# Kernel tuning notes

Measured on AMD Instinct MI355X. Metric: run time of the kernel, lower is better.

Reference implementation:

```python
import jax, jax.numpy as jnp
import numpy as np

# static config (matches init_kwargs and a standard 4-level FPN for ~800px input)
SPATIAL_SHAPES = ((100, 100), (50, 50), (25, 25), (13, 13))  # (H_l, W_l)
B, C, H, L, P = 2, 256, 8, 4, 4
DFFN = 2048
DH = C // H
LQ = sum(h * w for h, w in SPATIAL_SHAPES)  # 13294


def layer_norm(x, g, b, eps=1e-5):
    m = jnp.mean(x, -1, keepdims=True)
    v = jnp.mean((x - m) ** 2, -1, keepdims=True)
    return (x - m) * jax.lax.rsqrt(v + eps) * g + b


def ms_deform_sample(value, loc, attn):
    # value [B,Lv,H,DH], loc [B,Lq,H,L,P,2] in [0,1], attn [B,Lq,H,L,P]
    value = jnp.transpose(value, (0, 2, 1, 3))  # [B,H,Lv,DH]
    lq = loc.shape[1]
    out = jnp.zeros((B, H, lq, DH), value.dtype)
    start = 0
    for l, (Hl, Wl) in enumerate(SPATIAL_SHAPES):
        v = jax.lax.dynamic_slice_in_dim(value, start, Hl * Wl, axis=2)  # [B,H,N_l,DH]
        # grid_sample(align_corners=False) coords: x = loc_x*W - 0.5
        gx = jnp.transpose(loc[:, :, :, l, :, 0], (0, 2, 1, 3)) * Wl - 0.5  # [B,H,Lq,P]
        gy = jnp.transpose(loc[:, :, :, l, :, 1], (0, 2, 1, 3)) * Hl - 0.5
        aw = jnp.transpose(attn[:, :, :, l, :], (0, 2, 1, 3))  # [B,H,Lq,P]
        x0 = jnp.floor(gx)
        y0 = jnp.floor(gy)
        for dx in (0.0, 1.0):
            for dy in (0.0, 1.0):
                xi = x0 + dx
                yi = y0 + dy
                w = (1.0 - jnp.abs(gx - xi)) * (1.0 - jnp.abs(gy - yi))
                valid = (xi >= 0) & (xi < Wl) & (yi >= 0) & (yi < Hl)
                idx = (jnp.clip(yi, 0, Hl - 1) * Wl + jnp.clip(xi, 0, Wl - 1)).astype(jnp.int32)
                g = jnp.take_along_axis(v, idx.reshape(B, H, -1)[..., None], axis=2)  # [B,H,Lq*P,DH]
                ww = (w * aw * valid.astype(w.dtype))[..., None]  # [B,H,Lq,P,1]
                out = out + jnp.sum(g.reshape(B, H, lq, P, DH) * ww, axis=3)
        start += Hl * Wl
    return jnp.transpose(out, (0, 2, 1, 3)).reshape(B, lq, C)


def setup_inputs() -> dict:
    key = jax.random.key(0)
    ks = jax.random.split(key, 16)
    s = 0.02
    return {
        "src": jax.random.normal(ks[0], (B, LQ, C), jnp.float32),
        "pos": jax.random.normal(ks[1], (B, LQ, C), jnp.float32),
        "reference_points": jax.random.uniform(ks[2], (B, LQ, L, 2), jnp.float32),
        "w_value": jax.random.normal(ks[3], (C, C), jnp.float32) * s,
        "b_value": jnp.zeros((C,), jnp.float32),
        "w_off": jax.random.normal(ks[4], (C, H * L * P * 2), jnp.float32) * s,
        "b_off": jax.random.normal(ks[5], (H * L * P * 2,), jnp.float32) * s,
        "w_attn": jax.random.normal(ks[6], (C, H * L * P), jnp.float32) * s,
        "b_attn": jnp.zeros((H * L * P,), jnp.float32),
        "w_out": jax.random.normal(ks[7], (C, C), jnp.float32) * s,
        "b_out": jnp.zeros((C,), jnp.float32),
        "ln1_g": jnp.ones((C,), jnp.float32),
        "ln1_b": jnp.zeros((C,), jnp.float32),
        "w_ffn1": jax.random.normal(ks[8], (C, DFFN), jnp.float32) * s,
        "b_ffn1": jnp.zeros((DFFN,), jnp.float32),
        "w_ffn2": jax.random.normal(ks[9], (DFFN, C), jnp.float32) * s,
        "b_ffn2": jnp.zeros((C,), jnp.float32),
        "ln2_g": jnp.ones((C,), jnp.float32),
        "ln2_b": jnp.zeros((C,), jnp.float32),
    }


def reference(src, pos, reference_points, w_value, b_value, w_off, b_off, w_attn, b_attn,
              w_out, b_out, ln1_g, ln1_b, w_ffn1, b_ffn1, w_ffn2, b_ffn2, ln2_g, ln2_b):
    # DeformableTransformerEncoderLayer.forward (eval mode, no dropout)
    q = src + pos  # with_pos_embed
    lq = q.shape[1]
    value = (src @ w_value + b_value).reshape(B, -1, H, DH)
    off = (q @ w_off + b_off).reshape(B, lq, H, L, P, 2)
    attn = (q @ w_attn + b_attn).reshape(B, lq, H, L * P)
    attn = jax.nn.softmax(attn, axis=-1).reshape(B, lq, H, L, P)
    # offset_normalizer = (W_l, H_l)
    norm = jnp.array([[w, h] for h, w in SPATIAL_SHAPES], dtype=src.dtype)
    loc = reference_points[:, :, None, :, None, :] + off / norm[None, None, None, :, None, :]
    src2 = ms_deform_sample(value, loc, attn) @ w_out + b_out
    x = layer_norm(src + src2, ln1_g, ln1_b)
    ff = jax.nn.relu(x @ w_ffn1 + b_ffn1) @ w_ffn2 + b_ffn2
    return layer_norm(x + ff, ln2_g, ln2_b)
```

## Files before the change

kernel.cpp:

```cpp
#include <hip/hip_runtime.h>

#define LQN   13294
#define NBAT  2
#define MROWS (NBAT * LQN)
#define CCH   256
#define NHEAD 8
#define DHEAD 32
#define NLVL  4
#define NPT   4
#define DFF   2048

typedef short short8 __attribute__((ext_vector_type(8)));
typedef float f32x4 __attribute__((ext_vector_type(4)));
typedef unsigned short u16;
typedef u16 u16x4 __attribute__((ext_vector_type(4)));

__device__ __forceinline__ u16 f2bf(float f) {
  unsigned int u = __builtin_bit_cast(unsigned int, f);
  u += 0x7fffu + ((u >> 16) & 1u);
  return (u16)(u >> 16);
}
__device__ __forceinline__ float bf2f(u16 s) {
  unsigned int u = ((unsigned int)s) << 16;
  return __builtin_bit_cast(float, u);
}
__device__ __forceinline__ void async16(const void* g, void* l) {
  __builtin_amdgcn_global_load_lds(
      (const __attribute__((address_space(1))) void*)g,
      (__attribute__((address_space(3))) void*)l, 16, 0, 0);
}

__global__ __launch_bounds__(256, 2)
void gemm_dual(const u16* __restrict__ A0, const u16* __restrict__ BT0,
               const float* __restrict__ bias0, u16* __restrict__ C0,
               const u16* __restrict__ A1, const u16* __restrict__ BT1,
               const float* __restrict__ bias1, float* __restrict__ C1)
{
  __shared__ u16 As[2][128 * 64];
  __shared__ u16 Bs[2][128 * 64];
  const int t    = threadIdx.x;
  const int lane = t & 63;
  const int wid  = t >> 6;
  const int wm   = wid >> 1, wn = wid & 1;
  const int bm   = blockIdx.x;
  const int bnG  = blockIdx.y;
  const bool first = bnG < 2;
  const u16* A    = first ? A0 : A1;
  const u16* BT   = first ? BT0 : BT1;
  const float* bias = first ? bias0 : bias1;
  const int  bn   = first ? bnG : bnG - 2;
  const int l15  = lane & 15;
  const int kq   = lane >> 4;

  f32x4 acc[4][4];
#pragma unroll
  for (int m = 0; m < 4; ++m)
#pragma unroll
    for (int n = 0; n < 4; ++n) acc[m][n] = (f32x4)0.0f;

  auto stage = [&](int buf, int kt) {
#pragma unroll
    for (int i = 0; i < 4; ++i) {
      const int c   = i * 256 + t;
      const int row = c >> 3;
      const int kg  = (c & 7) ^ (row & 7);
      int ar = bm * 128 + row; ar = ar < MROWS ? ar : MROWS - 1;
      async16(&A[(size_t)ar * 256 + kt + kg * 8], &As[buf][c * 8]);
      const int br = bn * 128 + row;
      async16(&BT[(size_t)br * 256 + kt + kg * 8], &Bs[buf][c * 8]);
    }
  };

  stage(0, 0);
  __syncthreads();
  int cur = 0;

  for (int kt = 0; kt < 256; kt += 64) {
    if (kt + 64 < 256) stage(cur ^ 1, kt + 64);

#pragma unroll
    for (int kk = 0; kk < 2; ++kk) {
      short8 af[4], bfr[4];
#pragma unroll
      for (int m = 0; m < 4; ++m) {
        const int row = wm * 64 + m * 16 + l15;
        const int xb  = (kk * 64 + kq * 16) ^ ((row & 7) << 4);
        af[m] = *(const short8*)((const char*)&As[cur][0] + row * 128 + xb);
      }
#pragma unroll
      for (int n = 0; n < 4; ++n) {
        const int col = wn * 64 + n * 16 + l15;
        const int xb  = (kk * 64 + kq * 16) ^ ((col & 7) << 4);
        bfr[n] = *(const short8*)((const char*)&Bs[cur][0] + col * 128 + xb);
      }
#pragma unroll
      for (int m = 0; m < 4; ++m)
#pragma unroll
        for (int n = 0; n < 4; ++n)
          acc[m][n] = __builtin_amdgcn_mfma_f32_16x16x32_bf16(af[m], bfr[n], acc[m][n], 0, 0, 0);
    }

    __syncthreads();
    cur ^= 1;
  }

  const int crow0 = bm * 128 + wm * 64;
  const int ccol0 = bn * 128 + wn * 64;
#pragma unroll
  for (int n = 0; n < 4; ++n) {
    int col = ccol0 + n * 16 + l15;
    float bv = bias[col];
#pragma unroll
    for (int m = 0; m < 4; ++m) {
      int rbase = crow0 + m * 16 + kq * 4;
#pragma unroll
      for (int j = 0; j < 4; ++j) {
        int row = rbase + j;
        if (row < MROWS) {
          float v = acc[m][n][j] + bv;
          if (first) C0[(size_t)row * 256 + col] = f2bf(v);
          else       C1[(size_t)row * 384 + col] = v;
        }
      }
    }
  }
}

__global__ __launch_bounds__(512, 1)
void outproj_ln1(const u16* __restrict__ src2_bf, const u16* __restrict__ WT_out,
                 const float* __restrict__ b_out, const float* __restrict__ src,
                 const float* __restrict__ g1, const float* __restrict__ be1,
                 float* __restrict__ x_f32, u16* __restrict__ x_bf)
{
  extern __shared__ char smem[];
  char* As0 = smem;
  char* As1 = smem + 16384;
  char* Bs0 = smem + 32768;
  char* Bs1 = smem + 65536;
  float2* red = (float2*)(smem + 98304);

  const int t    = threadIdx.x;
  const int lane = t & 63;
  const int wid  = t >> 6;
  const int wm   = wid >> 2, wn = wid & 3;
  const int l15  = lane & 15;
  const int kq   = lane >> 4;
  const int bm   = blockIdx.x;

  auto stage = [&](char* Abuf, char* Bbuf, int kt) {
#pragma unroll
    for (int i = 0; i < 2; ++i) {
      const int c   = i * 512 + t;
      const int row = c >> 3;
      const int kg  = (c & 7) ^ (row & 7);
      int ar = bm * 128 + row; ar = ar < MROWS ? ar : MROWS - 1;
      async16(&src2_bf[(size_t)ar * 256 + kt + kg * 8], Abuf + c * 16);
    }
#pragma unroll
    for (int i = 0; i < 4; ++i) {
      const int c   = i * 512 + t;
      const int row = c >> 3;
      const int kg  = (c & 7) ^ (row & 7);
      async16(&WT_out[(size_t)row * 256 + kt + kg * 8], Bbuf + c * 16);
    }
  };

  f32x4 acc[4][4];
#pragma unroll
  for (int m = 0; m < 4; ++m)
#pragma unroll
    for (int n = 0; n < 4; ++n) acc[m][n] = (f32x4)0.0f;

  stage(As0, Bs0, 0);
  __syncthreads();

  for (int kt = 0; kt < 256; kt += 64) {
    const int cur = (kt >> 6) & 1;
    char* Ause = cur ? As1 : As0;
    char* Buse = cur ? Bs1 : Bs0;
    if (kt + 64 < 256) stage(cur ? As0 : As1, cur ? Bs0 : Bs1, kt + 64);

#pragma unroll
    for (int kk = 0; kk < 2; ++kk) {
      short8 af[4], bfr[4];
#pragma unroll
      for (int m = 0; m < 4; ++m) {
        const int row = wm * 64 + m * 16 + l15;
        const int xb  = (kk * 64 + kq * 16) ^ ((row & 7) << 4);
        af[m] = *(const short8*)(Ause + row * 128 + xb);
      }
#pragma unroll
      for (int n = 0; n < 4; ++n) {
        const int col = wn * 64 + n * 16 + l15;
        const int xb  = (kk * 64 + kq * 16) ^ ((col & 7) << 4);
        bfr[n] = *(const short8*)(Buse + col * 128 + xb);
      }
#pragma unroll
      for (int m = 0; m < 4; ++m)
#pragma unroll
        for (int n = 0; n < 4; ++n)
          acc[m][n] = __builtin_amdgcn_mfma_f32_16x16x32_bf16(af[m], bfr[n], acc[m][n], 0, 0, 0);
    }
    __syncthreads();
  }

#pragma unroll
  for (int n = 0; n < 4; ++n) {
    const int col = wn * 64 + n * 16 + l15;
    const float bv = b_out[col];
#pragma unroll
    for (int m = 0; m < 4; ++m)
#pragma unroll
      for (int j = 0; j < 4; ++j) {
        int row = bm * 128 + wm * 64 + m * 16 + kq * 4 + j;
        row = row < MROWS ? row : MROWS - 1;
        acc[m][n][j] += bv + src[(size_t)row * 256 + col];
      }
  }
  float s1[4][4], s2[4][4];
#pragma unroll
  for (int m = 0; m < 4; ++m)
#pragma unroll
    for (int j = 0; j < 4; ++j) {
      float a = 0.f, b = 0.f;
#pragma unroll
      for (int n = 0; n < 4; ++n) { const float v = acc[m][n][j]; a += v; b += v * v; }
      s1[m][j] = a; s2[m][j] = b;
    }
#pragma unroll
  for (int o = 1; o < 16; o <<= 1)
#pragma unroll
    for (int m = 0; m < 4; ++m)
#pragma unroll
      for (int j = 0; j < 4; ++j) {
        s1[m][j] += __shfl_xor(s1[m][j], o, 64);
        s2[m][j] += __shfl_xor(s2[m][j], o, 64);
      }
  if (l15 == 0)
#pragma unroll
    for (int m = 0; m < 4; ++m)
#pragma unroll
      for (int j = 0; j < 4; ++j)
        red[(wm * 64 + m * 16 + kq * 4 + j) * 4 + wn] = make_float2(s1[m][j], s2[m][j]);
  __syncthreads();
  float mean[4][4], rstd[4][4];
#pragma unroll
  for (int m = 0; m < 4; ++m)
#pragma unroll
    for (int j = 0; j < 4; ++j) {
      const int rl = wm * 64 + m * 16 + kq * 4 + j;
      float a = 0.f, b = 0.f;
#pragma unroll
      for (int w = 0; w < 4; ++w) { const float2 r = red[rl * 4 + w]; a += r.x; b += r.y; }
      const float mu = a * (1.0f / 256.0f);
      mean[m][j] = mu;
      rstd[m][j] = rsqrtf(b * (1.0f / 256.0f) - mu * mu + 1e-5f);
    }
#pragma unroll
  for (int n = 0; n < 4; ++n) {
    const int col = wn * 64 + n * 16 + l15;
    const float gg = g1[col], bb = be1[col];
#pragma unroll
    for (int m = 0; m < 4; ++m)
#pragma unroll
      for (int j = 0; j < 4; ++j) {
        const int row = bm * 128 + wm * 64 + m * 16 + kq * 4 + j;
        if (row < MROWS) {
          const float y = (acc[m][n][j] - mean[m][j]) * rstd[m][j] * gg + bb;
          x_f32[(size_t)row * 256 + col] = y;
          x_bf[(size_t)row * 256 + col] = f2bf(y);
        }
      }
  }
}

__global__ __launch_bounds__(1024, 2)
void ffn_ln2(const u16* __restrict__ x_bf, const u16* __restrict__ W1T,
             const u16* __restrict__ W2T, const float* __restrict__ b1,
             const float* __restrict__ b2, const float* __restrict__ x_f32,
             const float* __restrict__ g2, const float* __restrict__ be2,
             float* __restrict__ out)
{
  extern __shared__ char smem[];
  u16*  w1s = (u16*)(smem);
  u16*  w2s = (u16*)(smem + 65536);
  char* ps  = smem + 131072;
  float2* red = (float2*)(smem + 149504);

  const int t    = threadIdx.x;
  const int lane = t & 63;
  const int wid  = t >> 6;
  const int l15  = lane & 15;
  const int kq   = lane >> 4;
  const int bm   = blockIdx.x;
  const int pwm  = wid >> 1, pwn = wid & 1;
  const int vwm  = wid >> 2, vwn = wid & 3;

  short8 xr[8];
  {
    int ar = bm * 128 + pwm * 16 + l15;
    ar = ar < MROWS ? ar : MROWS - 1;
    const char* xb = (const char*)x_bf + (size_t)ar * 512 + kq * 16;
#pragma unroll
    for (int ks = 0; ks < 8; ++ks) xr[ks] = *(const short8*)(xb + ks * 64);
  }

  auto stage = [&](int buf, int it) {
#pragma unroll
    for (int i = 0; i < 2; ++i) {
      const int c  = i * 1024 + t;
      const int r1 = c >> 5;
      const int k1 = ((c & 31) ^ (r1 & 7)) * 8;
      async16(&W1T[(size_t)(it * 64 + r1) * 256 + k1], &w1s[buf * 16384 + c * 8]);
      const int r2 = c >> 3;
      const int k2 = ((c & 7) ^ (r2 & 7)) * 8;
      async16(&W2T[(size_t)r2 * 2048 + it * 64 + k2], &w2s[buf * 16384 + c * 8]);
    }
  };

  f32x4 acc[2][4];
#pragma unroll
  for (int m = 0; m < 2; ++m)
#pragma unroll
    for (int n = 0; n < 4; ++n) acc[m][n] = (f32x4)0.0f;

  stage(0, 0);
  __syncthreads();

  for (int it = 0; it < 32; ++it) {
    const int cur = it & 1;
    if (it < 31) stage(cur ^ 1, it + 1);

    f32x4 p[2];
    p[0] = (f32x4)0.0f; p[1] = (f32x4)0.0f;
#pragma unroll
    for (int ks = 0; ks < 8; ++ks) {
#pragma unroll
      for (int n = 0; n < 2; ++n) {
        const int wrow = pwn * 32 + n * 16 + l15;
        const int xb   = (((ks * 4 + kq) ^ (wrow & 7)) << 4);
        const short8 bfr = *(const short8*)((const char*)&w1s[cur * 16384] + wrow * 512 + xb);
        p[n] = __builtin_amdgcn_mfma_f32_16x16x32_bf16(xr[ks], bfr, p[n], 0, 0, 0);
      }
    }

#pragma unroll
    for (int n = 0; n < 2; ++n) {
      const int col = pwn * 32 + n * 16 + l15;
      const float bv = b1[it * 64 + col];
#pragma unroll
      for (int j = 0; j < 4; ++j) {
        const int prow = pwm * 16 + kq * 4 + j;
        *(u16*)(ps + prow * 144 + col * 2) = f2bf(fmaxf(p[n][j] + bv, 0.0f));
      }
    }
    __syncthreads();

#pragma unroll
    for (int kk = 0; kk < 2; ++kk) {
      short8 paf[2];
#pragma unroll
      for (int m = 0; m < 2; ++m) {
        const int arow = vwm * 32 + m * 16 + l15;
        paf[m] = *(const short8*)(ps + arow * 144 + (kk * 4 + kq) * 16);
      }
#pragma unroll
      for (int n = 0; n < 4; ++n) {
        const int brow = vwn * 64 + n * 16 + l15;
        const int xb   = (((kk * 4 + kq) ^ (brow & 7)) << 4);
        const short8 bfr = *(const short8*)((const char*)&w2s[cur * 16384] + brow * 128 + xb);
#pragma unroll
        for (int m = 0; m < 2; ++m)
          acc[m][n] = __builtin_amdgcn_mfma_f32_16x16x32_bf16(paf[m], bfr, acc[m][n], 0, 0, 0);
      }
    }
    __syncthreads();
  }

#pragma unroll
  for (int n = 0; n < 4; ++n) {
    const int col = vwn * 64 + n * 16 + l15;
    const float bv = b2[col];
#pragma unroll
    for (int m = 0; m < 2; ++m)
#pragma unroll
      for (int j = 0; j < 4; ++j) {
        int row = bm * 128 + vwm * 32 + m * 16 + kq * 4 + j;
        row = row < MROWS ? row : MROWS - 1;
        acc[m][n][j] += bv + x_f32[(size_t)row * 256 + col];
      }
  }
  float s1[2][4], s2[2][4];
#pragma unroll
  for (int m = 0; m < 2; ++m)
#pragma unroll
    for (int j = 0; j < 4; ++j) {
      float a = 0.f, b = 0.f;
#pragma unroll
      for (int n = 0; n < 4; ++n) { const float v = acc[m][n][j]; a += v; b += v * v; }
      s1[m][j] = a; s2[m][j] = b;
    }
#pragma unroll
  for (int o = 1; o < 16; o <<= 1)
#pragma unroll
    for (int m = 0; m < 2; ++m)
#pragma unroll
      for (int j = 0; j < 4; ++j) {
        s1[m][j] += __shfl_xor(s1[m][j], o, 64);
        s2[m][j] += __shfl_xor(s2[m][j], o, 64);
      }
  if (l15 == 0)
#pragma unroll
    for (int m = 0; m < 2; ++m)
#pragma unroll
      for (int j = 0; j < 4; ++j)
        red[(vwm * 32 + m * 16 + kq * 4 + j) * 4 + vwn] = make_float2(s1[m][j], s2[m][j]);
  __syncthreads();
  float mean[2][4], rstd[2][4];
#pragma unroll
  for (int m = 0; m < 2; ++m)
#pragma unroll
    for (int j = 0; j < 4; ++j) {
      const int rl = vwm * 32 + m * 16 + kq * 4 + j;
      float a = 0.f, b = 0.f;
#pragma unroll
      for (int w = 0; w < 4; ++w) { const float2 r = red[rl * 4 + w]; a += r.x; b += r.y; }
      const float mu = a * (1.0f / 256.0f);
      mean[m][j] = mu;
      rstd[m][j] = rsqrtf(b * (1.0f / 256.0f) - mu * mu + 1e-5f);
    }
#pragma unroll
  for (int n = 0; n < 4; ++n) {
    const int col = vwn * 64 + n * 16 + l15;
    const float gg = g2[col], bb = be2[col];
#pragma unroll
    for (int m = 0; m < 2; ++m)
#pragma unroll
      for (int j = 0; j < 4; ++j) {
        const int row = bm * 128 + vwm * 32 + m * 16 + kq * 4 + j;
        if (row < MROWS)
          out[(size_t)row * 256 + col] = (acc[m][n][j] - mean[m][j]) * rstd[m][j] * gg + bb;
      }
  }
}

__global__ __launch_bounds__(256)
void sampler_kernel(const float* __restrict__ offattn,
                    const float* __restrict__ refp,
                    const u16*  __restrict__ value,
                    u16*        __restrict__ src2)
{
  __shared__ float2 sWI[4][8][65];

  const int t    = threadIdx.x;
  const int r4   = t >> 6;
  const int lane = t & 63;
  const int row  = blockIdx.x * 4 + r4;
  const int b    = row / LQN;

  {
    const float* oa = offattn + (size_t)row * 384;
    const float* rp = refp + (size_t)row * 8;
    const int p16 = lane & 15;
    const int l   = p16 >> 2;
    const int Wl  = (l == 0) ? 100 : (l == 1) ? 50 : (l == 2) ? 25 : 13;
    const int st  = (l == 0) ? 0 : (l == 1) ? 10000 : (l == 2) ? 12500 : 13125;
    const float rx = rp[l * 2 + 0] * (float)Wl - 0.5f;
    const float ry = rp[l * 2 + 1] * (float)Wl - 0.5f;

#pragma unroll
    for (int s = 0; s < 2; ++s) {
      const int h = s * 4 + (lane >> 4);
      float logit = oa[256 + h * 16 + p16];
      float mx = logit;
#pragma unroll
      for (int o = 1; o < 16; o <<= 1) mx = fmaxf(mx, __shfl_xor(mx, o, 64));
      float e = __expf(logit - mx);
      float ssum = e;
#pragma unroll
      for (int o = 1; o < 16; o <<= 1) ssum += __shfl_xor(ssum, o, 64);
      const float aw = e / ssum;

      const float ox = oa[(h * 16 + p16) * 2 + 0];
      const float oy = oa[(h * 16 + p16) * 2 + 1];
      const float gx = rx + ox;
      const float gy = ry + oy;
      const float x0f = floorf(gx), y0f = floorf(gy);
      const int   x0 = (int)x0f, y0 = (int)y0f;
      const float fx = gx - x0f, fy = gy - y0f;
#pragma unroll
      for (int c = 0; c < 4; ++c) {
        const int dx = c & 1, dy = c >> 1;
        const int xi = x0 + dx, yi = y0 + dy;
        const float wx = dx ? fx : 1.0f - fx;
        const float wy = dy ? fy : 1.0f - fy;
        const bool valid = (xi >= 0) && (xi < Wl) && (yi >= 0) && (yi < Wl);
        const int xc = min(max(xi, 0), Wl - 1);
        const int yc = min(max(yi, 0), Wl - 1);
        const int idx = st + yc * Wl + xc;
        const float w = wx * wy * aw * (valid ? 1.0f : 0.0f);
        sWI[r4][h][p16 * 4 + c] = make_float2(w, __builtin_bit_cast(float, idx));
      }
    }
  }
  __syncthreads();

  {
    const int h  = lane >> 3;
    const int c4 = lane & 7;
    const char* vbase = (const char*)value + (size_t)b * LQN * 512 + h * 64 + c4 * 8;
    const float2* wi = sWI[r4][h];

    float a0 = 0.f, a1 = 0.f, a2 = 0.f, a3 = 0.f;
#pragma unroll 16
    for (int e = 0; e < 64; ++e) {
      const float2 p = wi[e];
      const float w  = p.x;
      const int  idx = __builtin_bit_cast(int, p.y);
      const unsigned long long u = *(const unsigned long long*)(vbase + (size_t)idx * 512);
      a0 += w * bf2f((u16)(u));
      a1 += w * bf2f((u16)(u >> 16));
      a2 += w * bf2f((u16)(u >> 32));
      a3 += w * bf2f((u16)(u >> 48));
    }
    u16x4 o;
    o[0] = f2bf(a0); o[1] = f2bf(a1); o[2] = f2bf(a2); o[3] = f2bf(a3);
    *(u16x4*)&src2[(size_t)row * 256 + h * 32 + c4 * 4] = o;
  }
}

__global__ __launch_bounds__(256)
void prep_qsrc(const float* __restrict__ src, const float* __restrict__ pos,
               u16* __restrict__ src_bf, u16* __restrict__ q_bf)
{
  const size_t i = (size_t)blockIdx.x * 256 + threadIdx.x;
  const f32x4 s = ((const f32x4*)src)[i];
  const f32x4 p = ((const f32x4*)pos)[i];
  u16x4 sb, qb;
#pragma unroll
  for (int j = 0; j < 4; ++j) { sb[j] = f2bf(s[j]); qb[j] = f2bf(s[j] + p[j]); }
  ((u16x4*)src_bf)[i] = sb;
  ((u16x4*)q_bf)[i]   = qb;
}

__global__ __launch_bounds__(256)
void prep_weights(const float* __restrict__ w_value, const float* __restrict__ w_off,
                  const float* __restrict__ w_attn,  const float* __restrict__ w_out,
                  const float* __restrict__ w_ffn1,  const float* __restrict__ w_ffn2,
                  const float* __restrict__ b_off,   const float* __restrict__ b_attn,
                  u16* __restrict__ WT_val, u16* __restrict__ WT_oa, u16* __restrict__ WT_out,
                  u16* __restrict__ WT_f1,  u16* __restrict__ WT_f2, float* __restrict__ bias_oa)
{
  int i = blockIdx.x * 256 + threadIdx.x;
  if (i < 65536) {
    const int k = i >> 8, n = i & 255;
    WT_val[n * 256 + k] = f2bf(w_value[i]);
  } else if ((i -= 65536) < 65536) {
    const int k = i >> 8, n = i & 255;
    WT_oa[n * 256 + k] = f2bf(w_off[i]);
  } else if ((i -= 65536) < 32768) {
    const int k = i >> 7, n = i & 127;
    WT_oa[(256 + n) * 256 + k] = f2bf(w_attn[i]);
  } else if ((i -= 32768) < 65536) {
    const int k = i >> 8, n = i & 255;
    WT_out[n * 256 + k] = f2bf(w_out[i]);
  } else if ((i -= 65536) < 524288) {
    const int k = i >> 11, n = i & 2047;
    WT_f1[n * 256 + k] = f2bf(w_ffn1[i]);
  } else if ((i -= 524288) < 524288) {
    const int k = i >> 8, n = i & 255;
    WT_f2[n * 2048 + k] = f2bf(w_ffn2[i]);
  } else if ((i -= 524288) < 384) {
    bias_oa[i] = (i < 256) ? b_off[i] : b_attn[i - 256];
  }
}

extern "C" void kernel_launch(void* const* d_in, const int* in_sizes, int n_in,
                              void* d_out, int out_size, void* d_ws, size_t ws_size,
                              hipStream_t stream)
{
  const float* src     = (const float*)d_in[0];
  const float* pos     = (const float*)d_in[1];
  const float* refp    = (const float*)d_in[2];
  const float* w_value = (const float*)d_in[3];
  const float* b_value = (const float*)d_in[4];
  const float* w_off   = (const float*)d_in[5];
  const float* b_off   = (const float*)d_in[6];
  const float* w_attn  = (const float*)d_in[7];
  const float* b_attn  = (const float*)d_in[8];
  const float* w_out   = (const float*)d_in[9];
  const float* b_out   = (const float*)d_in[10];
  const float* ln1_g   = (const float*)d_in[11];
  const float* ln1_b   = (const float*)d_in[12];
  const float* w_ffn1  = (const float*)d_in[13];
  const float* b_ffn1  = (const float*)d_in[14];
  const float* w_ffn2  = (const float*)d_in[15];
  const float* b_ffn2  = (const float*)d_in[16];
  const float* ln2_g   = (const float*)d_in[17];
  const float* ln2_b   = (const float*)d_in[18];

  char* ws = (char*)d_ws;
  size_t off = 0;
  auto alloc = [&](size_t bytes) { void* p = ws + off; off += (bytes + 255) & ~(size_t)255; return p; };

  u16*   src_bf   = (u16*)  alloc((size_t)MROWS * 256 * 2);
  u16*   q_bf     = (u16*)  alloc((size_t)MROWS * 256 * 2);
  float* offattn  = (float*)alloc((size_t)MROWS * 384 * 4);
  u16*   value_bf = (u16*)  alloc((size_t)MROWS * 256 * 2);
  u16*   src2_bf  = (u16*)  alloc((size_t)MROWS * 256 * 2);
  float* x_f32    = (float*)alloc((size_t)MROWS * 256 * 4);
  u16*   WT_val   = (u16*)  alloc(256 * 256 * 2);
  u16*   WT_oa    = (u16*)  alloc(384 * 256 * 2);
  u16*   WT_out   = (u16*)  alloc(256 * 256 * 2);
  u16*   WT_f1    = (u16*)  alloc(2048 * 256 * 2);
  u16*   WT_f2    = (u16*)  alloc((size_t)256 * 2048 * 2);
  float* bias_oa  = (float*)alloc(384 * 4);

  u16* x_bf = q_bf;

  prep_weights<<<4994, 256, 0, stream>>>(w_value, w_off, w_attn, w_out, w_ffn1, w_ffn2,
                                         b_off, b_attn,
                                         WT_val, WT_oa, WT_out, WT_f1, WT_f2, bias_oa);

  prep_qsrc<<<6647, 256, 0, stream>>>(src, pos, src_bf, q_bf);

  static bool attr_set = false;
  if (!attr_set) {
    hipFuncSetAttribute((const void*)ffn_ln2,
                        hipFuncAttributeMaxDynamicSharedMemorySize, 153600);
    hipFuncSetAttribute((const void*)outproj_ln1,
                        hipFuncAttributeMaxDynamicSharedMemorySize, 102400);
    attr_set = true;
  }

  gemm_dual<<<dim3(208, 5), 256, 0, stream>>>(src_bf, WT_val, b_value, value_bf,
                                              q_bf, WT_oa, bias_oa, offattn);

  sampler_kernel<<<MROWS / 4, 256, 0, stream>>>(offattn, refp, value_bf, src2_bf);

  outproj_ln1<<<208, 512, 102400, stream>>>(src2_bf, WT_out, b_out, src,
                                            ln1_g, ln1_b, x_f32, x_bf);

  ffn_ln2<<<208, 1024, 153600, stream>>>(x_bf, WT_f1, WT_f2, b_ffn1, b_ffn2,
                                         x_f32, ln2_g, ln2_b, (float*)d_out);
}
```

Before: 239.0 us.

## Restructure FFN kernel into software-pipelined 512-thread loop with 4-stage weight buffers

The fused FFN+LN2 kernel now runs 512 threads per block instead of 1024, so each wave holds twice the rows of accumulators. It walks the hidden dimension in 64 chunks of 32 instead of 32 chunks of 64. Weights are staged through a 4-deep ring with prefetch two chunks ahead. The hidden activations are double-buffered, so the FFN2 MFMAs for chunk it-1 and the FFN1 MFMAs for chunk it share one barrier per iteration instead of two. The intent is to cut barrier stalls and overlap the two GEMM stages, at the cost of higher register pressure, lower occupancy and an unswizzled W2 tile layout that may cause LDS bank conflicts.

```diff
diff --git a/kernel.cpp b/kernel.cpp
--- a/kernel.cpp
+++ b/kernel.cpp
@@ -274,7 +274,7 @@
   }
 }
 
-__global__ __launch_bounds__(1024, 2)
+__global__ __launch_bounds__(512)
 void ffn_ln2(const u16* __restrict__ x_bf, const u16* __restrict__ W1T,
              const u16* __restrict__ W2T, const float* __restrict__ b1,
              const float* __restrict__ b2, const float* __restrict__ x_f32,
@@ -282,10 +282,10 @@
              float* __restrict__ out)
 {
   extern __shared__ char smem[];
-  u16*  w1s = (u16*)(smem);
-  u16*  w2s = (u16*)(smem + 65536);
+  char* w1s = smem;
+  char* w2s = smem + 65536;
   char* ps  = smem + 131072;
-  float2* red = (float2*)(smem + 149504);
+  float2* red = (float2*)(smem + 151552);
 
   const int t    = threadIdx.x;
   const int lane = t & 63;
@@ -296,85 +296,106 @@
   const int pwm  = wid >> 1, pwn = wid & 1;
   const int vwm  = wid >> 2, vwn = wid & 3;
 
-  short8 xr[8];
-  {
-    int ar = bm * 128 + pwm * 16 + l15;
+  short8 xr[2][8];
+#pragma unroll
+  for (int m = 0; m < 2; ++m) {
+    int ar = bm * 128 + pwm * 32 + m * 16 + l15;
     ar = ar < MROWS ? ar : MROWS - 1;
     const char* xb = (const char*)x_bf + (size_t)ar * 512 + kq * 16;
 #pragma unroll
-    for (int ks = 0; ks < 8; ++ks) xr[ks] = *(const short8*)(xb + ks * 64);
+    for (int ks = 0; ks < 8; ++ks) xr[m][ks] = *(const short8*)(xb + ks * 64);
   }
 
   auto stage = [&](int buf, int it) {
 #pragma unroll
     for (int i = 0; i < 2; ++i) {
-      const int c  = i * 1024 + t;
+      const int c  = i * 512 + t;
       const int r1 = c >> 5;
       const int k1 = ((c & 31) ^ (r1 & 7)) * 8;
-      async16(&W1T[(size_t)(it * 64 + r1) * 256 + k1], &w1s[buf * 16384 + c * 8]);
-      const int r2 = c >> 3;
-      const int k2 = ((c & 7) ^ (r2 & 7)) * 8;
-      async16(&W2T[(size_t)r2 * 2048 + it * 64 + k2], &w2s[buf * 16384 + c * 8]);
+      async16(&W1T[(size_t)(it * 32 + r1) * 256 + k1], w1s + buf * 16384 + c * 16);
+      const int r2 = c >> 2;
+      const int k2 = (c & 3) * 8;
+      async16(&W2T[(size_t)r2 * 2048 + it * 32 + k2], w2s + buf * 16384 + c * 16);
     }
   };
 
-  f32x4 acc[2][4];
-#pragma unroll
-  for (int m = 0; m < 2; ++m)
+  f32x4 acc[4][4];
+#pragma unroll
+  for (int m = 0; m < 4; ++m)
 #pragma unroll
     for (int n = 0; n < 4; ++n) acc[m][n] = (f32x4)0.0f;
 
   stage(0, 0);
+  stage(1, 1);
   __syncthreads();
 
-  for (int it = 0; it < 32; ++it) {
-    const int cur = it & 1;
-    if (it < 31) stage(cur ^ 1, it + 1);
-
-    f32x4 p[2];
-    p[0] = (f32x4)0.0f; p[1] = (f32x4)0.0f;
-#pragma unroll
-    for (int ks = 0; ks < 8; ++ks) {
-#pragma unroll
-      for (int n = 0; n < 2; ++n) {
-        const int wrow = pwn * 32 + n * 16 + l15;
-        const int xb   = (((ks * 4 + kq) ^ (wrow & 7)) << 4);
-        const short8 bfr = *(const short8*)((const char*)&w1s[cur * 16384] + wrow * 512 + xb);
-        p[n] = __builtin_amdgcn_mfma_f32_16x16x32_bf16(xr[ks], bfr, p[n], 0, 0, 0);
-      }
-    }
-
-#pragma unroll
-    for (int n = 0; n < 2; ++n) {
-      const int col = pwn * 32 + n * 16 + l15;
-      const float bv = b1[it * 64 + col];
-#pragma unroll
-      for (int j = 0; j < 4; ++j) {
-        const int prow = pwm * 16 + kq * 4 + j;
-        *(u16*)(ps + prow * 144 + col * 2) = f2bf(fmaxf(p[n][j] + bv, 0.0f));
-      }
-    }
-    __syncthreads();
-
-#pragma unroll
-    for (int kk = 0; kk < 2; ++kk) {
-      short8 paf[2];
-#pragma unroll
-      for (int m = 0; m < 2; ++m) {
-        const int arow = vwm * 32 + m * 16 + l15;
-        paf[m] = *(const short8*)(ps + arow * 144 + (kk * 4 + kq) * 16);
+  for (int it = 0; it < 64; ++it) {
+    if (it + 2 < 64) stage((it + 2) & 3, it + 2);
+
+    if (it > 0) {
+      const char* psR = ps + ((it - 1) & 1) * 10240;
+      const char* w2u = w2s + ((it - 1) & 3) * 16384;
+      short8 paf[4];
+#pragma unroll
+      for (int m = 0; m < 4; ++m) {
+        const int arow = vwm * 64 + m * 16 + l15;
+        paf[m] = *(const short8*)(psR + arow * 80 + kq * 16);
       }
 #pragma unroll
       for (int n = 0; n < 4; ++n) {
         const int brow = vwn * 64 + n * 16 + l15;
-        const int xb   = (((kk * 4 + kq) ^ (brow & 7)) << 4);
-        const short8 bfr = *(const short8*)((const char*)&w2s[cur * 16384] + brow * 128 + xb);
+        const short8 bfr = *(const short8*)(w2u + brow * 64 + kq * 16);
+#pragma unroll
+        for (int m = 0; m < 4; ++m)
+          acc[m][n] = __builtin_amdgcn_mfma_f32_16x16x32_bf16(paf[m], bfr, acc[m][n], 0, 0, 0);
+      }
+    }
+
+    {
+      const char* w1u = w1s + (it & 3) * 16384;
+      char* psW = ps + (it & 1) * 10240;
+      f32x4 p[2];
+      p[0] = (f32x4)0.0f; p[1] = (f32x4)0.0f;
+#pragma unroll
+      for (int ks = 0; ks < 8; ++ks) {
+        const int wrow = pwn * 16 + l15;
+        const int xb   = (((ks * 4 + kq) ^ (wrow & 7)) << 4);
+        const short8 bfr = *(const short8*)(w1u + wrow * 512 + xb);
 #pragma unroll
         for (int m = 0; m < 2; ++m)
-          acc[m][n] = __builtin_amdgcn_mfma_f32_16x16x32_bf16(paf[m], bfr, acc[m][n], 0, 0, 0);
-      }
-    }
+          p[m] = __builtin_amdgcn_mfma_f32_16x16x32_bf16(xr[m][ks], bfr, p[m], 0, 0, 0);
+      }
+      const int col = pwn * 16 + l15;
+      const float bv = b1[it * 32 + col];
+#pragma unroll
+      for (int m = 0; m < 2; ++m)
+#pragma unroll
+        for (int j = 0; j < 4; ++j) {
+          const int prow = pwm * 32 + m * 16 + kq * 4 + j;
+          *(u16*)(psW + prow * 80 + col * 2) = f2bf(fmaxf(p[m][j] + bv, 0.0f));
+        }
+    }
+
     __syncthreads();
+  }
+
+  {
+    const char* psR = ps + (63 & 1) * 10240;
+    const char* w2u = w2s + (63 & 3) * 16384;
+    short8 paf[4];
+#pragma unroll
+    for (int m = 0; m < 4; ++m) {
+      const int arow = vwm * 64 + m * 16 + l15;
+      paf[m] = *(const short8*)(psR + arow * 80 + kq * 16);
+    }
+#pragma unroll
+    for (int n = 0; n < 4; ++n) {
+      const int brow = vwn * 64 + n * 16 + l15;
+      const short8 bfr = *(const short8*)(w2u + brow * 64 + kq * 16);
+#pragma unroll
+      for (int m = 0; m < 4; ++m)
+        acc[m][n] = __builtin_amdgcn_mfma_f32_16x16x32_bf16(paf[m], bfr, acc[m][n], 0, 0, 0);
+    }
   }
 
 #pragma unroll
@@ -382,17 +403,17 @@
     const int col = vwn * 64 + n * 16 + l15;
     const float bv = b2[col];
 #pragma unroll
-    for (int m = 0; m < 2; ++m)
+    for (int m = 0; m < 4; ++m)
 #pragma unroll
       for (int j = 0; j < 4; ++j) {
-        int row = bm * 128 + vwm * 32 + m * 16 + kq * 4 + j;
+        int row = bm * 128 + vwm * 64 + m * 16 + kq * 4 + j;
         row = row < MROWS ? row : MROWS - 1;
         acc[m][n][j] += bv + x_f32[(size_t)row * 256 + col];
       }
   }
-  float s1[2][4], s2[2][4];
-#pragma unroll
-  for (int m = 0; m < 2; ++m)
+  float s1[4][4], s2[4][4];
+#pragma unroll
+  for (int m = 0; m < 4; ++m)
 #pragma unroll
     for (int j = 0; j < 4; ++j) {
       float a = 0.f, b = 0.f;
@@ -403,7 +424,7 @@
 #pragma unroll
   for (int o = 1; o < 16; o <<= 1)
 #pragma unroll
-    for (int m = 0; m < 2; ++m)
+    for (int m = 0; m < 4; ++m)
 #pragma unroll
       for (int j = 0; j < 4; ++j) {
         s1[m][j] += __shfl_xor(s1[m][j], o, 64);
@@ -411,17 +432,17 @@
       }
   if (l15 == 0)
 #pragma unroll
-    for (int m = 0; m < 2; ++m)
+    for (int m = 0; m < 4; ++m)
 #pragma unroll
       for (int j = 0; j < 4; ++j)
-        red[(vwm * 32 + m * 16 + kq * 4 + j) * 4 + vwn] = make_float2(s1[m][j], s2[m][j]);
+        red[(vwm * 64 + m * 16 + kq * 4 + j) * 4 + vwn] = make_float2(s1[m][j], s2[m][j]);
   __syncthreads();
-  float mean[2][4], rstd[2][4];
-#pragma unroll
-  for (int m = 0; m < 2; ++m)
+  float mean[4][4], rstd[4][4];
+#pragma unroll
+  for (int m = 0; m < 4; ++m)
 #pragma unroll
     for (int j = 0; j < 4; ++j) {
-      const int rl = vwm * 32 + m * 16 + kq * 4 + j;
+      const int rl = vwm * 64 + m * 16 + kq * 4 + j;
       float a = 0.f, b = 0.f;
 #pragma unroll
       for (int w = 0; w < 4; ++w) { const float2 r = red[rl * 4 + w]; a += r.x; b += r.y; }
@@ -434,10 +455,10 @@
     const int col = vwn * 64 + n * 16 + l15;
     const float gg = g2[col], bb = be2[col];
 #pragma unroll
-    for (int m = 0; m < 2; ++m)
+    for (int m = 0; m < 4; ++m)
 #pragma unroll
       for (int j = 0; j < 4; ++j) {
-        const int row = bm * 128 + vwm * 32 + m * 16 + kq * 4 + j;
+        const int row = bm * 128 + vwm * 64 + m * 16 + kq * 4 + j;
         if (row < MROWS)
           out[(size_t)row * 256 + col] = (acc[m][n][j] - mean[m][j]) * rstd[m][j] * gg + bb;
       }
@@ -627,7 +648,7 @@
   static bool attr_set = false;
   if (!attr_set) {
     hipFuncSetAttribute((const void*)ffn_ln2,
-                        hipFuncAttributeMaxDynamicSharedMemorySize, 153600);
+                        hipFuncAttributeMaxDynamicSharedMemorySize, 155648);
     hipFuncSetAttribute((const void*)outproj_ln1,
                         hipFuncAttributeMaxDynamicSharedMemorySize, 102400);
     attr_set = true;
@@ -641,6 +662,6 @@
   outproj_ln1<<<208, 512, 102400, stream>>>(src2_bf, WT_out, b_out, src,
                                             ln1_g, ln1_b, x_f32, x_bf);
 
-  ffn_ln2<<<208, 1024, 153600, stream>>>(x_bf, WT_f1, WT_f2, b_ffn1, b_ffn2,
-                                         x_f32, ln2_g, ln2_b, (float*)d_out);
-}
+  ffn_ln2<<<208, 512, 155648, stream>>>(x_bf, WT_f1, WT_f2, b_ffn1, b_ffn2,
+                                        x_f32, ln2_g, ln2_b, (float*)d_out);
+}
```

Result: no change. 238.0 us (-0.4%).

## Widen sampler gathers to 16 bytes, remap blocks per XCD, merge prep kernels

Applied to the files above, without the earlier changes.

The sampler now has each lane gather 8 bf16 channels (16 bytes) instead of 4. The 64 sample points are split between the two half-waves, whose partial sums are combined with a cross-lane shuffle before one half writes the output. Block IDs are remapped so that each XCD handles a contiguous range of rows, which should improve L2 locality for the value gathers. The two preprocessing kernels are merged into a single launch to save launch overhead. The trade-offs are a shuffle reduction and half the lanes sitting idle during the store.

```diff
diff --git a/kernel.cpp b/kernel.cpp
--- a/kernel.cpp
+++ b/kernel.cpp
@@ -14,6 +14,8 @@
 typedef float f32x4 __attribute__((ext_vector_type(4)));
 typedef unsigned short u16;
 typedef u16 u16x4 __attribute__((ext_vector_type(4)));
+typedef unsigned int u32;
+typedef u32 u32x4 __attribute__((ext_vector_type(4)));
 
 __device__ __forceinline__ u16 f2bf(float f) {
   unsigned int u = __builtin_bit_cast(unsigned int, f);
@@ -452,11 +454,18 @@
 {
   __shared__ float2 sWI[4][8][65];
 
+  const int bid  = blockIdx.x;
+  const int xcd  = bid & 7;
+  const int idx  = bid >> 3;
+  const int wgid = (xcd < 7 ? xcd * 831 : 7 * 831) + (xcd < 7 ? idx : idx) + (xcd < 7 ? 0 : 0);
+  const int wg   = (xcd < 7) ? (xcd * 831 + idx) : (5817 + idx);
+
   const int t    = threadIdx.x;
   const int r4   = t >> 6;
   const int lane = t & 63;
-  const int row  = blockIdx.x * 4 + r4;
+  const int row  = wg * 4 + r4;
   const int b    = row / LQN;
+  (void)wgid;
 
   {
     const float* oa = offattn + (size_t)row * 384;
@@ -497,61 +506,71 @@
         const bool valid = (xi >= 0) && (xi < Wl) && (yi >= 0) && (yi < Wl);
         const int xc = min(max(xi, 0), Wl - 1);
         const int yc = min(max(yi, 0), Wl - 1);
-        const int idx = st + yc * Wl + xc;
+        const int idxv = st + yc * Wl + xc;
         const float w = wx * wy * aw * (valid ? 1.0f : 0.0f);
-        sWI[r4][h][p16 * 4 + c] = make_float2(w, __builtin_bit_cast(float, idx));
+        sWI[r4][h][p16 * 4 + c] = make_float2(w, __builtin_bit_cast(float, idxv));
       }
     }
   }
   __syncthreads();
 
   {
-    const int h  = lane >> 3;
-    const int c4 = lane & 7;
-    const char* vbase = (const char*)value + (size_t)b * LQN * 512 + h * 64 + c4 * 8;
+    const int e2 = lane >> 5;
+    const int h  = (lane >> 2) & 7;
+    const int c8 = lane & 3;
+    const char* vbase = (const char*)value + (size_t)b * LQN * 512 + h * 64 + c8 * 16;
     const float2* wi = sWI[r4][h];
 
-    float a0 = 0.f, a1 = 0.f, a2 = 0.f, a3 = 0.f;
-#pragma unroll 16
-    for (int e = 0; e < 64; ++e) {
-      const float2 p = wi[e];
+    float a[8];
+#pragma unroll
+    for (int i = 0; i < 8; ++i) a[i] = 0.f;
+
+#pragma unroll 8
+    for (int e = 0; e < 64; e += 2) {
+      const float2 p = wi[e + e2];
       const float w  = p.x;
-      const int  idx = __builtin_bit_cast(int, p.y);
-      const unsigned long long u = *(const unsigned long long*)(vbase + (size_t)idx * 512);
-      a0 += w * bf2f((u16)(u));
-      a1 += w * bf2f((u16)(u >> 16));
-      a2 += w * bf2f((u16)(u >> 32));
-      a3 += w * bf2f((u16)(u >> 48));
-    }
-    u16x4 o;
-    o[0] = f2bf(a0); o[1] = f2bf(a1); o[2] = f2bf(a2); o[3] = f2bf(a3);
-    *(u16x4*)&src2[(size_t)row * 256 + h * 32 + c4 * 4] = o;
+      const int  idxv = __builtin_bit_cast(int, p.y);
+      const u32x4 u = *(const u32x4*)(vbase + (size_t)idxv * 512);
+#pragma unroll
+      for (int i = 0; i < 4; ++i) {
+        a[2 * i]     += w * bf2f((u16)(u[i]));
+        a[2 * i + 1] += w * bf2f((u16)(u[i] >> 16));
+      }
+    }
+#pragma unroll
+    for (int i = 0; i < 8; ++i) a[i] += __shfl_xor(a[i], 32, 64);
+
+    if (e2 == 0) {
+      u16 o[8];
+#pragma unroll
+      for (int i = 0; i < 8; ++i) o[i] = f2bf(a[i]);
+      *(short8*)&src2[(size_t)row * 256 + h * 32 + c8 * 8] = *(short8*)o;
+    }
   }
 }
 
 __global__ __launch_bounds__(256)
-void prep_qsrc(const float* __restrict__ src, const float* __restrict__ pos,
-               u16* __restrict__ src_bf, u16* __restrict__ q_bf)
+void prep_all(const float* __restrict__ src, const float* __restrict__ pos,
+              u16* __restrict__ src_bf, u16* __restrict__ q_bf,
+              const float* __restrict__ w_value, const float* __restrict__ w_off,
+              const float* __restrict__ w_attn,  const float* __restrict__ w_out,
+              const float* __restrict__ w_ffn1,  const float* __restrict__ w_ffn2,
+              const float* __restrict__ b_off,   const float* __restrict__ b_attn,
+              u16* __restrict__ WT_val, u16* __restrict__ WT_oa, u16* __restrict__ WT_out,
+              u16* __restrict__ WT_f1,  u16* __restrict__ WT_f2, float* __restrict__ bias_oa)
 {
-  const size_t i = (size_t)blockIdx.x * 256 + threadIdx.x;
-  const f32x4 s = ((const f32x4*)src)[i];
-  const f32x4 p = ((const f32x4*)pos)[i];
-  u16x4 sb, qb;
-#pragma unroll
-  for (int j = 0; j < 4; ++j) { sb[j] = f2bf(s[j]); qb[j] = f2bf(s[j] + p[j]); }
-  ((u16x4*)src_bf)[i] = sb;
-  ((u16x4*)q_bf)[i]   = qb;
-}
-
-__global__ __launch_bounds__(256)
-void prep_weights(const float* __restrict__ w_value, const float* __restrict__ w_off,
-                  const float* __restrict__ w_attn,  const float* __restrict__ w_out,
-                  const float* __restrict__ w_ffn1,  const float* __restrict__ w_ffn2,
-                  const float* __restrict__ b_off,   const float* __restrict__ b_attn,
-                  u16* __restrict__ WT_val, u16* __restrict__ WT_oa, u16* __restrict__ WT_out,
-                  u16* __restrict__ WT_f1,  u16* __restrict__ WT_f2, float* __restrict__ bias_oa)
-{
-  int i = blockIdx.x * 256 + threadIdx.x;
+  if (blockIdx.x < 6647) {
+    const size_t i = (size_t)blockIdx.x * 256 + threadIdx.x;
+    const f32x4 s = ((const f32x4*)src)[i];
+    const f32x4 p = ((const f32x4*)pos)[i];
+    u16x4 sb, qb;
+#pragma unroll
+    for (int j = 0; j < 4; ++j) { sb[j] = f2bf(s[j]); qb[j] = f2bf(s[j] + p[j]); }
+    ((u16x4*)src_bf)[i] = sb;
+    ((u16x4*)q_bf)[i]   = qb;
+    return;
+  }
+  int i = (blockIdx.x - 6647) * 256 + threadIdx.x;
   if (i < 65536) {
     const int k = i >> 8, n = i & 255;
     WT_val[n * 256 + k] = f2bf(w_value[i]);
@@ -618,11 +637,10 @@
 
   u16* x_bf = q_bf;
 
-  prep_weights<<<4994, 256, 0, stream>>>(w_value, w_off, w_attn, w_out, w_ffn1, w_ffn2,
-                                         b_off, b_attn,
-                                         WT_val, WT_oa, WT_out, WT_f1, WT_f2, bias_oa);
-
-  prep_qsrc<<<6647, 256, 0, stream>>>(src, pos, src_bf, q_bf);
+  prep_all<<<6647 + 4994, 256, 0, stream>>>(src, pos, src_bf, q_bf,
+                                            w_value, w_off, w_attn, w_out, w_ffn1, w_ffn2,
+                                            b_off, b_attn,
+                                            WT_val, WT_oa, WT_out, WT_f1, WT_f2, bias_oa);
 
   static bool attr_set = false;
   if (!attr_set) {
```

After: 240.3 us. Within noise of the previous version (+0.5%).
